# Kernel optimization log

Measured on AMD Instinct MI355X. Metric: run time of the kernel, lower is better.

Reference implementation:

```python
import jax, jax.numpy as jnp
import numpy as np

B, TT, TS, H, O = 16, 512, 512, 1024, 1024


def setup_inputs() -> dict:
    key = jax.random.key(0)
    k1, k2, k3, k4, k5 = jax.random.split(key, 5)
    ht = jax.random.normal(k1, (B, TT, H), dtype=jnp.float32)
    hs = jax.random.normal(k2, (B, TS, H), dtype=jnp.float32)
    source = jax.random.randint(k3, (B, TS), 0, 10000, dtype=jnp.int32)
    # glorot-like scaling for weights
    W_a = jax.random.normal(k4, (H, H), dtype=jnp.float32) * (2.0 / (H + H)) ** 0.5
    W_c = jax.random.normal(k5, (2 * H, O), dtype=jnp.float32) * (2.0 / (2 * H + O)) ** 0.5
    b = jnp.zeros((O,), dtype=jnp.float32)
    return {"ht": ht, "hs": hs, "source": source, "W_a": W_a, "W_c": W_c, "b": b}


def reference(ht, hs, source, W_a, W_c, b):
    # score = ht . (hs @ W_a)^T : [B, Tt, Ts]
    keys = jnp.einsum('bsk,kl->bsl', hs, W_a)
    score = jnp.einsum('btk,bsk->bts', ht, keys)
    # stable exp with max subtraction (matches original manual softmax)
    score = jnp.exp(score - jnp.max(score, axis=-1, keepdims=True))
    # sequence mask from count of non-pad (non-zero) source tokens
    lens = jnp.sum((source != 0).astype(jnp.int32), axis=1)          # [B]
    mask = (jnp.arange(TS)[None, :] < lens[:, None]).astype(score.dtype)  # [B, Ts]
    score = score * mask[:, None, :]
    a = score / jnp.sum(score, axis=-1, keepdims=True)               # [B, Tt, Ts]
    c = jnp.einsum('bts,bsk->btk', a, hs)                            # context [B, Tt, H]
    h = jnp.concatenate([c, ht], axis=-1)                            # [B, Tt, 2H]
    return jnp.tanh(jnp.einsum('btk,kl->btl', h, W_c) + b)
```

## Files before the change

### kernel.cpp

```cpp
#include <hip/hip_runtime.h>
#include <math.h>

typedef unsigned short u16;
typedef unsigned int u32;

using f32x4 = __attribute__((ext_vector_type(4))) float;
using f16x8 = __attribute__((ext_vector_type(8))) _Float16;
using u32x4 = __attribute__((ext_vector_type(4))) u32;

#define DEVI static __device__ __forceinline__

#define BB 16
#define TT 512
#define TS 512
#define HH 1024
#define OO 1024

#define LO_SCALE 2048.0f
#define LO_INV 4.8828125e-4f

DEVI void split1h(float x, u16& hb, u16& lb) {
    _Float16 h = (_Float16)x;
    _Float16 l = (_Float16)((x - (float)h) * LO_SCALE);
    hb = __builtin_bit_cast(u16, h);
    lb = __builtin_bit_cast(u16, l);
}

DEVI float h2f(u16 b) { return (float)__builtin_bit_cast(_Float16, b); }

DEVI void gl16(const void* g, void* l) {
    __builtin_amdgcn_global_load_lds(
        (__attribute__((address_space(1))) const void*)g,
        (__attribute__((address_space(3))) void*)l, 16, 0, 0);
}

__global__ void lens_kernel(const int* __restrict__ src, int* __restrict__ lens) {
    int b = blockIdx.x;
    int v = (src[b * TS + (int)threadIdx.x] != 0) ? 1 : 0;
    unsigned long long m = __ballot(v);
    __shared__ int part[8];
    if ((threadIdx.x & 63) == 0) part[threadIdx.x >> 6] = __popcll(m);
    __syncthreads();
    if (threadIdx.x == 0) {
        int s = 0;
#pragma unroll
        for (int i = 0; i < 8; ++i) s += part[i];
        lens[b] = s;
    }
}

__global__ void transpose_split_kernel(const float* __restrict__ src,
                                       u16* __restrict__ dhi, u16* __restrict__ dlo,
                                       int R, int C) {
    __shared__ float tile[32][33];
    long boff = (long)blockIdx.z * R * C;
    src += boff;
    dhi += boff;
    if (dlo) dlo += boff;
    int c0 = blockIdx.x * 32, r0 = blockIdx.y * 32;
    int tx = threadIdx.x, ty = threadIdx.y;
#pragma unroll
    for (int i = 0; i < 32; i += 8)
        tile[ty + i][tx] = src[(long)(r0 + ty + i) * C + (c0 + tx)];
    __syncthreads();
#pragma unroll
    for (int i = 0; i < 32; i += 8) {
        u16 hb, lb;
        split1h(tile[tx][ty + i], hb, lb);
        long o = (long)(c0 + ty + i) * R + (r0 + tx);
        dhi[o] = hb;
        if (dlo) dlo[o] = lb;
    }
}

__global__ void softmax_mask_kernel(u16* __restrict__ hi, u16* __restrict__ lo,
                                    const int* __restrict__ lens) {
    long row = blockIdx.x;
    int len = lens[blockIdx.x >> 9];
    u16* ph = hi + row * TS;
    u16* pl = lo + row * TS;
    int lane = threadIdx.x;
    f16x8 vh = *(const f16x8*)(ph + 8 * lane);
    f16x8 vl = *(const f16x8*)(pl + 8 * lane);
    float f[8];
#pragma unroll
    for (int i = 0; i < 8; ++i) f[i] = (float)vh[i] + (float)vl[i] * LO_INV;
    float m = f[0];
#pragma unroll
    for (int i = 1; i < 8; ++i) m = fmaxf(m, f[i]);
#pragma unroll
    for (int o = 32; o > 0; o >>= 1) m = fmaxf(m, __shfl_xor(m, o));
    float e[8];
    float sum = 0.f;
#pragma unroll
    for (int i = 0; i < 8; ++i) {
        e[i] = (8 * lane + i < len) ? expf(f[i] - m) : 0.f;
        sum += e[i];
    }
#pragma unroll
    for (int o = 32; o > 0; o >>= 1) sum += __shfl_xor(sum, o);
    float inv = 1.0f / sum;
#pragma unroll
    for (int i = 0; i < 8; ++i) vh[i] = (_Float16)(e[i] * inv);
    *(f16x8*)(ph + 8 * lane) = vh;
}

template <int ASRC, int EPI, int TERMS, bool SWZ>
__global__ __launch_bounds__(256, 2)
void gemm_h(const u16* __restrict__ Ahi, const u16* __restrict__ Alo,
            const float* __restrict__ Af,
            const u16* __restrict__ Bhi, const u16* __restrict__ Blo,
            float* __restrict__ C, u16* __restrict__ Chi, u16* __restrict__ Clo,
            const float* __restrict__ bias,
            int M, int N, int K,
            long sA, long sB, long sC) {
    int bx, by, bz;
    if (SWZ) {
        int id = blockIdx.x;
        int ns = ((id & 7) << 6) | (id >> 3);
        bx = ns & 7;
        by = ns >> 3;
        bz = 0;
    } else {
        bx = blockIdx.x;
        by = blockIdx.y;
        bz = blockIdx.z;
    }
    if (ASRC == 0) {
        Ahi += (long)bz * sA;
        if (TERMS == 3) Alo += (long)bz * sA;
    } else if (ASRC == 1) {
        Af += (long)bz * sA;
    }
    Bhi += (long)bz * sB;
    if (TERMS == 3) Blo += (long)bz * sB;

    int n0 = bx * 128;
    int m0 = by * 128;

    constexpr int NARR = (TERMS == 3) ? 4 : 2;
    constexpr int AH = 0;
    constexpr int AL = 1;
    constexpr int BH = (TERMS == 3) ? 2 : 1;
    constexpr int BL = 3;
    __shared__ u16 lds[2][NARR * 4096];

    int tid = threadIdx.x;
    int lane = tid & 63;
    int wave = tid >> 6;
    int wm = (wave >> 1) * 64;
    int wn = (wave & 1) * 64;
    int fr = lane & 15;
    int kq = lane >> 4;

    const int lda = (ASRC == 2) ? HH : K;

    f32x4 acc[4][4];
    f32x4 acc2[TERMS == 3 ? 4 : 1][TERMS == 3 ? 4 : 1];
#pragma unroll
    for (int i = 0; i < 4; ++i)
#pragma unroll
        for (int j = 0; j < 4; ++j) acc[i][j] = (f32x4){0.f, 0.f, 0.f, 0.f};
    if (TERMS == 3) {
#pragma unroll
        for (int i = 0; i < 4; ++i)
#pragma unroll
            for (int j = 0; j < 4; ++j) acc2[i][j] = (f32x4){0.f, 0.f, 0.f, 0.f};
    }

    auto stage_gl = [&](int bufi, int arr, const u16* g, int r0, int ldg, int k0) {
#pragma unroll
        for (int h = 0; h < 2; ++h) {
            int vt = tid + h * 256;
            int row = vt >> 2;
            int ls = (vt & 3) ^ ((row >> 1) & 3);
            const u16* gp = g + (long)(r0 + row) * ldg + (k0 + 8 * ls);
            u16* lp = &lds[bufi][arr * 4096 + (vt >> 6) * 512];
            gl16(gp, lp);
        }
    };

    auto stage_a_f32 = [&](int bufi, const float* g, int ldg, int kk) {
        int r = tid >> 1;
        int hf = (tid & 1) * 16;
        const float* p = g + (long)(m0 + r) * ldg + kk + hf;
        float4 a0 = *(const float4*)(p + 0);
        float4 a1 = *(const float4*)(p + 4);
        float4 a2 = *(const float4*)(p + 8);
        float4 a3 = *(const float4*)(p + 12);
        float fv[16] = {a0.x, a0.y, a0.z, a0.w, a1.x, a1.y, a1.z, a1.w,
                        a2.x, a2.y, a2.z, a2.w, a3.x, a3.y, a3.z, a3.w};
        u16 hb[16], lb[16];
#pragma unroll
        for (int i = 0; i < 16; ++i) split1h(fv[i], hb[i], lb[i]);
        int sw = (r >> 1) & 3;
        int ls0 = hf >> 3;
        u32x4 h0 = {(u32)hb[0] | ((u32)hb[1] << 16), (u32)hb[2] | ((u32)hb[3] << 16),
                    (u32)hb[4] | ((u32)hb[5] << 16), (u32)hb[6] | ((u32)hb[7] << 16)};
        u32x4 h1 = {(u32)hb[8] | ((u32)hb[9] << 16), (u32)hb[10] | ((u32)hb[11] << 16),
                    (u32)hb[12] | ((u32)hb[13] << 16), (u32)hb[14] | ((u32)hb[15] << 16)};
        u16* ah = &lds[bufi][AH * 4096 + r * 32];
        *(u32x4*)(ah + (((ls0 + 0) ^ sw) << 3)) = h0;
        *(u32x4*)(ah + (((ls0 + 1) ^ sw) << 3)) = h1;
        if (TERMS == 3) {
            u32x4 l0 = {(u32)lb[0] | ((u32)lb[1] << 16), (u32)lb[2] | ((u32)lb[3] << 16),
                        (u32)lb[4] | ((u32)lb[5] << 16), (u32)lb[6] | ((u32)lb[7] << 16)};
            u32x4 l1 = {(u32)lb[8] | ((u32)lb[9] << 16), (u32)lb[10] | ((u32)lb[11] << 16),
                        (u32)lb[12] | ((u32)lb[13] << 16), (u32)lb[14] | ((u32)lb[15] << 16)};
            u16* al = &lds[bufi][AL * 4096 + r * 32];
            *(u32x4*)(al + (((ls0 + 0) ^ sw) << 3)) = l0;
            *(u32x4*)(al + (((ls0 + 1) ^ sw) << 3)) = l1;
        }
    };

    auto stage = [&](int bufi, int t) {
        int k0 = t * 32;
        stage_gl(bufi, BH, Bhi, n0, K, k0);
        if (TERMS == 3) stage_gl(bufi, BL, Blo, n0, K, k0);
        if (ASRC == 0) {
            stage_gl(bufi, AH, Ahi, m0, lda, k0);
            if (TERMS == 3) stage_gl(bufi, AL, Alo, m0, lda, k0);
        } else if (ASRC == 1) {
            stage_a_f32(bufi, Af, lda, k0);
        } else {
            if (k0 < HH)
                stage_gl(bufi, AH, Ahi, m0, HH, k0);
            else
                stage_a_f32(bufi, Af, HH, k0 - HH);
        }
    };

    const int NT = K / 32;
    stage(0, 0);
    __syncthreads();
    int cur = 0;
    for (int t = 0; t < NT; ++t) {
        if (t + 1 < NT) stage(cur ^ 1, t + 1);

        const u16* L = lds[cur];
        f16x8 afh[4], afl[4], bfh[4], bfl[4];
#pragma unroll
        for (int i = 0; i < 4; ++i) {
            int ra = wm + i * 16 + fr;
            int rb = wn + i * 16 + fr;
            int oa = ra * 32 + ((kq ^ ((ra >> 1) & 3)) << 3);
            int ob = rb * 32 + ((kq ^ ((rb >> 1) & 3)) << 3);
            afh[i] = *(const f16x8*)(L + AH * 4096 + oa);
            bfh[i] = *(const f16x8*)(L + BH * 4096 + ob);
            if (TERMS == 3) {
                afl[i] = *(const f16x8*)(L + AL * 4096 + oa);
                bfl[i] = *(const f16x8*)(L + BL * 4096 + ob);
            }
        }
#pragma unroll
        for (int i = 0; i < 4; ++i)
#pragma unroll
            for (int j = 0; j < 4; ++j) {
                acc[i][j] = __builtin_amdgcn_mfma_f32_16x16x32_f16(afh[i], bfh[j], acc[i][j], 0, 0, 0);
                if (TERMS == 3) {
                    acc2[i][j] = __builtin_amdgcn_mfma_f32_16x16x32_f16(afl[i], bfh[j], acc2[i][j], 0, 0, 0);
                    acc2[i][j] = __builtin_amdgcn_mfma_f32_16x16x32_f16(afh[i], bfl[j], acc2[i][j], 0, 0, 0);
                }
            }
        __syncthreads();
        cur ^= 1;
    }

    int fq = (lane >> 4) * 4;
#pragma unroll
    for (int i = 0; i < 4; ++i)
#pragma unroll
        for (int j = 0; j < 4; ++j)
#pragma unroll
            for (int g = 0; g < 4; ++g) {
                int row = m0 + wm + i * 16 + fq + g;
                int col = n0 + wn + j * 16 + fr;
                long idx = (long)bz * sC + (long)row * N + col;
                float v = acc[i][j][g];
                if (TERMS == 3) v += acc2[i][j][g] * LO_INV;
                if constexpr (EPI == 1) {
                    u16 h2, l2;
                    split1h(v, h2, l2);
                    Chi[idx] = h2;
                    Clo[idx] = l2;
                } else if constexpr (EPI == 2) {
                    float x = v + bias[col];
                    float t2 = __expf(2.f * x);
                    C[idx] = 1.f - 2.f * __builtin_amdgcn_rcpf(t2 + 1.f);
                } else {
                    Chi[idx] = __builtin_bit_cast(u16, (_Float16)v);
                }
            }
}

extern "C" void kernel_launch(void* const* d_in, const int* in_sizes, int n_in,
                              void* d_out, int out_size, void* d_ws, size_t ws_size,
                              hipStream_t stream) {
    const float* ht = (const float*)d_in[0];
    const float* hs = (const float*)d_in[1];
    const int* source = (const int*)d_in[2];
    const float* Wa = (const float*)d_in[3];
    const float* Wc = (const float*)d_in[4];
    const float* bias = (const float*)d_in[5];
    float* out = (float*)d_out;

    char* w = (char*)d_ws;
    size_t off = 0;
    auto alloc = [&](size_t bytes) -> void* {
        void* p = w + off;
        off += (bytes + 255) & ~(size_t)255;
        return p;
    };
    int* lens = (int*)alloc(256);
    u16* keysHi = (u16*)alloc((size_t)BB * TS * HH * 2);
    u16* keysLo = (u16*)alloc((size_t)BB * TS * HH * 2);
    u16* scoreHi = (u16*)alloc((size_t)BB * TT * TS * 2);
    u16* scoreLo = (u16*)alloc((size_t)BB * TT * TS * 2);
    u16* hsTHi = (u16*)alloc((size_t)BB * HH * TS * 2);
    u16* WaTHi = (u16*)alloc((size_t)HH * HH * 2);
    u16* WaTLo = (u16*)alloc((size_t)HH * HH * 2);
    u16* cHi = keysHi;
    u16* WcTHi = scoreLo;

    lens_kernel<<<BB, TS, 0, stream>>>(source, lens);
    transpose_split_kernel<<<dim3(HH / 32, HH / 32, 1), dim3(32, 8), 0, stream>>>(
        Wa, WaTHi, WaTLo, HH, HH);
    transpose_split_kernel<<<dim3(HH / 32, TS / 32, BB), dim3(32, 8), 0, stream>>>(
        hs, hsTHi, nullptr, TS, HH);

    gemm_h<1, 1, 3, true><<<dim3(512), 256, 0, stream>>>(
        nullptr, nullptr, hs, WaTHi, WaTLo,
        nullptr, keysHi, keysLo, nullptr,
        BB * TS, HH, HH, 0, 0, 0);

    gemm_h<1, 1, 3, false><<<dim3(TS / 128, TT / 128, BB), 256, 0, stream>>>(
        nullptr, nullptr, ht, keysHi, keysLo,
        nullptr, scoreHi, scoreLo, nullptr,
        TT, TS, HH, (long)TT * HH, (long)TS * HH, (long)TT * TS);

    softmax_mask_kernel<<<BB * TT, 64, 0, stream>>>(scoreHi, scoreLo, lens);

    gemm_h<0, 3, 1, false><<<dim3(HH / 128, TT / 128, BB), 256, 0, stream>>>(
        scoreHi, nullptr, nullptr, hsTHi, nullptr,
        nullptr, cHi, nullptr, nullptr,
        TT, HH, TS, (long)TT * TS, (long)HH * TS, (long)TT * HH);

    transpose_split_kernel<<<dim3(OO / 32, 2 * HH / 32, 1), dim3(32, 8), 0, stream>>>(
        Wc, WcTHi, nullptr, 2 * HH, OO);

    gemm_h<2, 2, 1, true><<<dim3(512), 256, 0, stream>>>(
        cHi, nullptr, ht, WcTHi, nullptr,
        out, nullptr, nullptr, bias,
        BB * TT, OO, 2 * HH, 0, 0, 0);
}
```

Before: 216.8 us.

## Switch split-precision GEMMs to bf16 hi/lo and split-K the score GEMM

Replaces the scaled fp16 hi/lo split with a bf16 hi/lo split for the keys and score GEMMs, so all three MFMA terms accumulate into a single accumulator instead of two. This cuts accumulator registers, which may help occupancy or scheduling. The score GEMM is also split along K into two halves launched as separate blocks, doubling the grid, and the softmax kernel sums the four partial bf16 hi/lo buffers. The trade-off is extra memory traffic for the partial score buffers, plus some accuracy risk from bf16's shorter mantissa.

```diff
diff --git a/kernel.cpp b/kernel.cpp
--- a/kernel.cpp
+++ b/kernel.cpp
@@ -5,6 +5,7 @@
 typedef unsigned int u32;
 
 using f32x4 = __attribute__((ext_vector_type(4))) float;
+using s16x8 = __attribute__((ext_vector_type(8))) short;
 using f16x8 = __attribute__((ext_vector_type(8))) _Float16;
 using u32x4 = __attribute__((ext_vector_type(4))) u32;
 
@@ -16,17 +17,25 @@
 #define HH 1024
 #define OO 1024
 
-#define LO_SCALE 2048.0f
-#define LO_INV 4.8828125e-4f
-
-DEVI void split1h(float x, u16& hb, u16& lb) {
-    _Float16 h = (_Float16)x;
-    _Float16 l = (_Float16)((x - (float)h) * LO_SCALE);
-    hb = __builtin_bit_cast(u16, h);
-    lb = __builtin_bit_cast(u16, l);
-}
-
-DEVI float h2f(u16 b) { return (float)__builtin_bit_cast(_Float16, b); }
+DEVI void split_bf(float x, u16& hb, u16& lb) {
+    u32 xb = __float_as_uint(x);
+    float hf = __uint_as_float(xb & 0xffff0000u);
+    hb = (u16)(xb >> 16);
+    lb = (u16)(__float_as_uint(x - hf) >> 16);
+}
+
+DEVI float ub(u16 h) { return __uint_as_float((u32)h << 16); }
+
+template <int PREC> struct FragT;
+template <> struct FragT<0> { using T = s16x8; };
+template <> struct FragT<1> { using T = f16x8; };
+
+DEVI f32x4 mfma16(s16x8 a, s16x8 b, f32x4 c) {
+    return __builtin_amdgcn_mfma_f32_16x16x32_bf16(a, b, c, 0, 0, 0);
+}
+DEVI f32x4 mfma16(f16x8 a, f16x8 b, f32x4 c) {
+    return __builtin_amdgcn_mfma_f32_16x16x32_f16(a, b, c, 0, 0, 0);
+}
 
 DEVI void gl16(const void* g, void* l) {
     __builtin_amdgcn_global_load_lds(
@@ -49,6 +58,7 @@
     }
 }
 
+template <int PREC>
 __global__ void transpose_split_kernel(const float* __restrict__ src,
                                        u16* __restrict__ dhi, u16* __restrict__ dlo,
                                        int R, int C) {
@@ -56,7 +66,7 @@
     long boff = (long)blockIdx.z * R * C;
     src += boff;
     dhi += boff;
-    if (dlo) dlo += boff;
+    if (PREC == 0) dlo += boff;
     int c0 = blockIdx.x * 32, r0 = blockIdx.y * 32;
     int tx = threadIdx.x, ty = threadIdx.y;
 #pragma unroll
@@ -65,31 +75,39 @@
     __syncthreads();
 #pragma unroll
     for (int i = 0; i < 32; i += 8) {
-        u16 hb, lb;
-        split1h(tile[tx][ty + i], hb, lb);
+        float v = tile[tx][ty + i];
         long o = (long)(c0 + ty + i) * R + (r0 + tx);
-        dhi[o] = hb;
-        if (dlo) dlo[o] = lb;
-    }
-}
-
-__global__ void softmax_mask_kernel(u16* __restrict__ hi, u16* __restrict__ lo,
+        if constexpr (PREC == 0) {
+            u16 hb, lb;
+            split_bf(v, hb, lb);
+            dhi[o] = hb;
+            dlo[o] = lb;
+        } else {
+            dhi[o] = __builtin_bit_cast(u16, (_Float16)v);
+        }
+    }
+}
+
+__global__ void softmax_mask_kernel(u16* __restrict__ h0, u16* __restrict__ l0,
+                                    const u16* __restrict__ h1, const u16* __restrict__ l1,
                                     const int* __restrict__ lens) {
     long row = blockIdx.x;
     int len = lens[blockIdx.x >> 9];
-    u16* ph = hi + row * TS;
-    u16* pl = lo + row * TS;
     int lane = threadIdx.x;
-    f16x8 vh = *(const f16x8*)(ph + 8 * lane);
-    f16x8 vl = *(const f16x8*)(pl + 8 * lane);
+    long o = row * TS + 8 * lane;
+    s16x8 vh0 = *(const s16x8*)(h0 + o);
+    s16x8 vl0 = *(const s16x8*)(l0 + o);
+    s16x8 vh1 = *(const s16x8*)(h1 + o);
+    s16x8 vl1 = *(const s16x8*)(l1 + o);
     float f[8];
 #pragma unroll
-    for (int i = 0; i < 8; ++i) f[i] = (float)vh[i] + (float)vl[i] * LO_INV;
+    for (int i = 0; i < 8; ++i)
+        f[i] = (ub((u16)vh0[i]) + ub((u16)vl0[i])) + (ub((u16)vh1[i]) + ub((u16)vl1[i]));
     float m = f[0];
 #pragma unroll
     for (int i = 1; i < 8; ++i) m = fmaxf(m, f[i]);
 #pragma unroll
-    for (int o = 32; o > 0; o >>= 1) m = fmaxf(m, __shfl_xor(m, o));
+    for (int os = 32; os > 0; os >>= 1) m = fmaxf(m, __shfl_xor(m, os));
     float e[8];
     float sum = 0.f;
 #pragma unroll
@@ -98,22 +116,23 @@
         sum += e[i];
     }
 #pragma unroll
-    for (int o = 32; o > 0; o >>= 1) sum += __shfl_xor(sum, o);
+    for (int os = 32; os > 0; os >>= 1) sum += __shfl_xor(sum, os);
     float inv = 1.0f / sum;
-#pragma unroll
-    for (int i = 0; i < 8; ++i) vh[i] = (_Float16)(e[i] * inv);
-    *(f16x8*)(ph + 8 * lane) = vh;
-}
-
-template <int ASRC, int EPI, int TERMS, bool SWZ>
+    f16x8 p;
+#pragma unroll
+    for (int i = 0; i < 8; ++i) p[i] = (_Float16)(e[i] * inv);
+    *(f16x8*)(h0 + o) = p;
+}
+
+template <int PREC, int ASRC, int EPI, int TERMS, int KSPLIT, bool SWZ>
 __global__ __launch_bounds__(256, 2)
-void gemm_h(const u16* __restrict__ Ahi, const u16* __restrict__ Alo,
+void gemm_u(const u16* __restrict__ Ahi, const u16* __restrict__ Alo,
             const float* __restrict__ Af,
             const u16* __restrict__ Bhi, const u16* __restrict__ Blo,
             float* __restrict__ C, u16* __restrict__ Chi, u16* __restrict__ Clo,
             const float* __restrict__ bias,
-            int M, int N, int K,
-            long sA, long sB, long sC) {
+            int M, int N, int K, int lda, int ldb,
+            long sA, long sB, long sC, long sKh) {
     int bx, by, bz;
     if (SWZ) {
         int id = blockIdx.x;
@@ -126,21 +145,25 @@
         by = blockIdx.y;
         bz = blockIdx.z;
     }
+    int kh = 0;
+    if (KSPLIT == 2) {
+        kh = bz & 1;
+        bz >>= 1;
+    }
     if (ASRC == 0) {
-        Ahi += (long)bz * sA;
-        if (TERMS == 3) Alo += (long)bz * sA;
+        Ahi += (long)bz * sA + (long)kh * K;
+        if (TERMS == 3) Alo += (long)bz * sA + (long)kh * K;
     } else if (ASRC == 1) {
-        Af += (long)bz * sA;
-    }
-    Bhi += (long)bz * sB;
-    if (TERMS == 3) Blo += (long)bz * sB;
+        Af += (long)bz * sA + (long)kh * K;
+    }
+    Bhi += (long)bz * sB + (long)kh * K;
+    if (TERMS == 3) Blo += (long)bz * sB + (long)kh * K;
 
     int n0 = bx * 128;
     int m0 = by * 128;
 
     constexpr int NARR = (TERMS == 3) ? 4 : 2;
-    constexpr int AH = 0;
-    constexpr int AL = 1;
+    constexpr int AH = 0, AL = 1;
     constexpr int BH = (TERMS == 3) ? 2 : 1;
     constexpr int BL = 3;
     __shared__ u16 lds[2][NARR * 4096];
@@ -153,20 +176,11 @@
     int fr = lane & 15;
     int kq = lane >> 4;
 
-    const int lda = (ASRC == 2) ? HH : K;
-
     f32x4 acc[4][4];
-    f32x4 acc2[TERMS == 3 ? 4 : 1][TERMS == 3 ? 4 : 1];
 #pragma unroll
     for (int i = 0; i < 4; ++i)
 #pragma unroll
         for (int j = 0; j < 4; ++j) acc[i][j] = (f32x4){0.f, 0.f, 0.f, 0.f};
-    if (TERMS == 3) {
-#pragma unroll
-        for (int i = 0; i < 4; ++i)
-#pragma unroll
-            for (int j = 0; j < 4; ++j) acc2[i][j] = (f32x4){0.f, 0.f, 0.f, 0.f};
-    }
 
     auto stage_gl = [&](int bufi, int arr, const u16* g, int r0, int ldg, int k0) {
 #pragma unroll
@@ -192,7 +206,12 @@
                         a2.x, a2.y, a2.z, a2.w, a3.x, a3.y, a3.z, a3.w};
         u16 hb[16], lb[16];
 #pragma unroll
-        for (int i = 0; i < 16; ++i) split1h(fv[i], hb[i], lb[i]);
+        for (int i = 0; i < 16; ++i) {
+            if constexpr (PREC == 0)
+                split_bf(fv[i], hb[i], lb[i]);
+            else
+                hb[i] = __builtin_bit_cast(u16, (_Float16)fv[i]);
+        }
         int sw = (r >> 1) & 3;
         int ls0 = hf >> 3;
         u32x4 h0 = {(u32)hb[0] | ((u32)hb[1] << 16), (u32)hb[2] | ((u32)hb[3] << 16),
@@ -202,7 +221,7 @@
         u16* ah = &lds[bufi][AH * 4096 + r * 32];
         *(u32x4*)(ah + (((ls0 + 0) ^ sw) << 3)) = h0;
         *(u32x4*)(ah + (((ls0 + 1) ^ sw) << 3)) = h1;
-        if (TERMS == 3) {
+        if constexpr (TERMS == 3) {
             u32x4 l0 = {(u32)lb[0] | ((u32)lb[1] << 16), (u32)lb[2] | ((u32)lb[3] << 16),
                         (u32)lb[4] | ((u32)lb[5] << 16), (u32)lb[6] | ((u32)lb[7] << 16)};
             u32x4 l1 = {(u32)lb[8] | ((u32)lb[9] << 16), (u32)lb[10] | ((u32)lb[11] << 16),
@@ -215,8 +234,8 @@
 
     auto stage = [&](int bufi, int t) {
         int k0 = t * 32;
-        stage_gl(bufi, BH, Bhi, n0, K, k0);
-        if (TERMS == 3) stage_gl(bufi, BL, Blo, n0, K, k0);
+        stage_gl(bufi, BH, Bhi, n0, ldb, k0);
+        if (TERMS == 3) stage_gl(bufi, BL, Blo, n0, ldb, k0);
         if (ASRC == 0) {
             stage_gl(bufi, AH, Ahi, m0, lda, k0);
             if (TERMS == 3) stage_gl(bufi, AL, Alo, m0, lda, k0);
@@ -224,9 +243,9 @@
             stage_a_f32(bufi, Af, lda, k0);
         } else {
             if (k0 < HH)
-                stage_gl(bufi, AH, Ahi, m0, HH, k0);
+                stage_gl(bufi, AH, Ahi, m0, lda, k0);
             else
-                stage_a_f32(bufi, Af, HH, k0 - HH);
+                stage_a_f32(bufi, Af, lda, k0 - HH);
         }
     };
 
@@ -234,38 +253,40 @@
     stage(0, 0);
     __syncthreads();
     int cur = 0;
+    using FT = typename FragT<PREC>::T;
     for (int t = 0; t < NT; ++t) {
         if (t + 1 < NT) stage(cur ^ 1, t + 1);
 
         const u16* L = lds[cur];
-        f16x8 afh[4], afl[4], bfh[4], bfl[4];
+        FT afh[4], afl[4], bfh[4], bfl[4];
 #pragma unroll
         for (int i = 0; i < 4; ++i) {
             int ra = wm + i * 16 + fr;
             int rb = wn + i * 16 + fr;
             int oa = ra * 32 + ((kq ^ ((ra >> 1) & 3)) << 3);
             int ob = rb * 32 + ((kq ^ ((rb >> 1) & 3)) << 3);
-            afh[i] = *(const f16x8*)(L + AH * 4096 + oa);
-            bfh[i] = *(const f16x8*)(L + BH * 4096 + ob);
+            afh[i] = *(const FT*)(L + AH * 4096 + oa);
+            bfh[i] = *(const FT*)(L + BH * 4096 + ob);
             if (TERMS == 3) {
-                afl[i] = *(const f16x8*)(L + AL * 4096 + oa);
-                bfl[i] = *(const f16x8*)(L + BL * 4096 + ob);
+                afl[i] = *(const FT*)(L + AL * 4096 + oa);
+                bfl[i] = *(const FT*)(L + BL * 4096 + ob);
             }
         }
 #pragma unroll
         for (int i = 0; i < 4; ++i)
 #pragma unroll
             for (int j = 0; j < 4; ++j) {
-                acc[i][j] = __builtin_amdgcn_mfma_f32_16x16x32_f16(afh[i], bfh[j], acc[i][j], 0, 0, 0);
+                acc[i][j] = mfma16(afh[i], bfh[j], acc[i][j]);
                 if (TERMS == 3) {
-                    acc2[i][j] = __builtin_amdgcn_mfma_f32_16x16x32_f16(afl[i], bfh[j], acc2[i][j], 0, 0, 0);
-                    acc2[i][j] = __builtin_amdgcn_mfma_f32_16x16x32_f16(afh[i], bfl[j], acc2[i][j], 0, 0, 0);
+                    acc[i][j] = mfma16(afl[i], bfh[j], acc[i][j]);
+                    acc[i][j] = mfma16(afh[i], bfl[j], acc[i][j]);
                 }
             }
         __syncthreads();
         cur ^= 1;
     }
 
+    long obase = (long)bz * sC + (long)kh * sKh;
     int fq = (lane >> 4) * 4;
 #pragma unroll
     for (int i = 0; i < 4; ++i)
@@ -275,12 +296,11 @@
             for (int g = 0; g < 4; ++g) {
                 int row = m0 + wm + i * 16 + fq + g;
                 int col = n0 + wn + j * 16 + fr;
-                long idx = (long)bz * sC + (long)row * N + col;
+                long idx = obase + (long)row * N + col;
                 float v = acc[i][j][g];
-                if (TERMS == 3) v += acc2[i][j][g] * LO_INV;
                 if constexpr (EPI == 1) {
                     u16 h2, l2;
-                    split1h(v, h2, l2);
+                    split_bf(v, h2, l2);
                     Chi[idx] = h2;
                     Clo[idx] = l2;
                 } else if constexpr (EPI == 2) {
@@ -314,42 +334,47 @@
     int* lens = (int*)alloc(256);
     u16* keysHi = (u16*)alloc((size_t)BB * TS * HH * 2);
     u16* keysLo = (u16*)alloc((size_t)BB * TS * HH * 2);
-    u16* scoreHi = (u16*)alloc((size_t)BB * TT * TS * 2);
-    u16* scoreLo = (u16*)alloc((size_t)BB * TT * TS * 2);
+    u16* scoreH0 = (u16*)alloc((size_t)BB * TT * TS * 2);
+    u16* scoreH1 = (u16*)alloc((size_t)BB * TT * TS * 2);
+    u16* scoreL0 = (u16*)alloc((size_t)BB * TT * TS * 2);
+    u16* scoreL1 = (u16*)alloc((size_t)BB * TT * TS * 2);
     u16* hsTHi = (u16*)alloc((size_t)BB * HH * TS * 2);
     u16* WaTHi = (u16*)alloc((size_t)HH * HH * 2);
     u16* WaTLo = (u16*)alloc((size_t)HH * HH * 2);
     u16* cHi = keysHi;
-    u16* WcTHi = scoreLo;
+    u16* WcTHi = scoreL0;
+    u16* prob = scoreH0;
 
     lens_kernel<<<BB, TS, 0, stream>>>(source, lens);
-    transpose_split_kernel<<<dim3(HH / 32, HH / 32, 1), dim3(32, 8), 0, stream>>>(
+    transpose_split_kernel<0><<<dim3(HH / 32, HH / 32, 1), dim3(32, 8), 0, stream>>>(
         Wa, WaTHi, WaTLo, HH, HH);
-    transpose_split_kernel<<<dim3(HH / 32, TS / 32, BB), dim3(32, 8), 0, stream>>>(
+    transpose_split_kernel<1><<<dim3(HH / 32, TS / 32, BB), dim3(32, 8), 0, stream>>>(
         hs, hsTHi, nullptr, TS, HH);
 
-    gemm_h<1, 1, 3, true><<<dim3(512), 256, 0, stream>>>(
+    gemm_u<0, 1, 1, 3, 1, true><<<dim3(512), 256, 0, stream>>>(
         nullptr, nullptr, hs, WaTHi, WaTLo,
         nullptr, keysHi, keysLo, nullptr,
-        BB * TS, HH, HH, 0, 0, 0);
-
-    gemm_h<1, 1, 3, false><<<dim3(TS / 128, TT / 128, BB), 256, 0, stream>>>(
+        BB * TS, HH, HH, HH, HH, 0, 0, 0, 0);
+
+    gemm_u<0, 1, 1, 3, 2, false><<<dim3(TS / 128, TT / 128, 2 * BB), 256, 0, stream>>>(
         nullptr, nullptr, ht, keysHi, keysLo,
-        nullptr, scoreHi, scoreLo, nullptr,
-        TT, TS, HH, (long)TT * HH, (long)TS * HH, (long)TT * TS);
-
-    softmax_mask_kernel<<<BB * TT, 64, 0, stream>>>(scoreHi, scoreLo, lens);
-
-    gemm_h<0, 3, 1, false><<<dim3(HH / 128, TT / 128, BB), 256, 0, stream>>>(
-        scoreHi, nullptr, nullptr, hsTHi, nullptr,
+        nullptr, scoreH0, scoreL0, nullptr,
+        TT, TS, HH / 2, HH, HH,
+        (long)TT * HH, (long)TS * HH, (long)TT * TS, (long)BB * TT * TS);
+
+    softmax_mask_kernel<<<BB * TT, 64, 0, stream>>>(scoreH0, scoreL0, scoreH1, scoreL1, lens);
+
+    gemm_u<1, 0, 3, 1, 1, false><<<dim3(HH / 128, TT / 128, BB), 256, 0, stream>>>(
+        prob, nullptr, nullptr, hsTHi, nullptr,
         nullptr, cHi, nullptr, nullptr,
-        TT, HH, TS, (long)TT * TS, (long)HH * TS, (long)TT * HH);
-
-    transpose_split_kernel<<<dim3(OO / 32, 2 * HH / 32, 1), dim3(32, 8), 0, stream>>>(
+        TT, HH, TS, TS, TS,
+        (long)TT * TS, (long)HH * TS, (long)TT * HH, 0);
+
+    transpose_split_kernel<1><<<dim3(OO / 32, 2 * HH / 32, 1), dim3(32, 8), 0, stream>>>(
         Wc, WcTHi, nullptr, 2 * HH, OO);
 
-    gemm_h<2, 2, 1, true><<<dim3(512), 256, 0, stream>>>(
+    gemm_u<1, 2, 2, 1, 1, true><<<dim3(512), 256, 0, stream>>>(
         cHi, nullptr, ht, WcTHi, nullptr,
         out, nullptr, nullptr, bias,
-        BB * TT, OO, 2 * HH, 0, 0, 0);
-}
+        BB * TT, OO, 2 * HH, HH, 2 * HH, 0, 0, 0, 0);
+}
```

Result: faster. 196.4 us (-9.4%).
